# Performance work log

Measured on AMD Instinct MI355X. Metric: run time of the kernel, lower is better.

The kernel has to match this reference:

```python
import jax, jax.numpy as jnp
import numpy as np

EPS = 1e-9
TOP_K = 2


def setup_inputs() -> dict:
    key = jax.random.key(0)
    k = jax.random.split(key, 6)
    B, E, D_IN, D_MODEL, D_SEL = 16384, 8, 900, 512, 128
    return {
        "cycle_curve_data": jax.random.normal(k[0], (B, D_IN), jnp.float32),
        "logits": jax.random.normal(k[1], (B, E), jnp.float32),
        "moe_masks": jax.random.randint(k[2], (B, E), 0, 2, jnp.int32),
        "selection_embeddings": jax.random.normal(k[3], (B, E, D_SEL), jnp.float32),
        "W": jax.random.normal(k[4], (E, D_IN, D_MODEL), jnp.float32) / np.sqrt(D_IN).astype(np.float32),
        "b": jnp.zeros((E, D_MODEL), jnp.float32),
    }


def reference(cycle_curve_data, logits, moe_masks, selection_embeddings, W, b):
    B, E = logits.shape
    mask = (moe_masks == 1).astype(logits.dtype)  # [B, E]
    raw = jax.nn.softmax(logits, axis=1)          # [B, E]

    # inactive-expert mixture for selection embedding
    inactive = raw * (1.0 - mask)
    inactive = inactive / (jnp.sum(inactive, axis=1, keepdims=True) + EPS)
    selection_embedding = jnp.einsum("bes,be->bs", selection_embeddings, inactive)

    # active gates + top-k selection + renormalization
    active = raw * mask
    _, idx = jax.lax.top_k(active, TOP_K)                                  # [B, K]
    top_mask = jnp.sum(jax.nn.one_hot(idx, E, dtype=active.dtype), axis=1)  # [B, E]
    gates = active * top_mask
    gates = gates / (jnp.sum(gates, axis=1, keepdims=True) + EPS)

    # dense formulation of dispatch -> per-expert Linear -> weighted combine:
    # out[b] = sum_e gates[b,e] * (x[b] @ W[e] + b[e])
    expert_out = jnp.einsum("bd,edm->bem", cycle_curve_data, W) + b  # [B, E, D_model]
    final_out = jnp.einsum("bem,be->bm", expert_out, gates).astype(jnp.bfloat16)

    # guide loss (training-mode auxiliary loss)
    s = jnp.sum(raw * mask) / B
    guide_loss = (1.0 - s) * (1.0 - s)
    return final_out, guide_loss, selection_embedding
```

## Files before the change

### kernel.cpp

```cpp
#include <hip/hip_runtime.h>
#include <hip/hip_bf16.h>


#define B_ROWS 16384
#define DIN 900
#define DM 512
#define DSEL 128
#define KP 928
#define NKS 29
#define MAXT 192
#define EPSF 1e-9f

#define OUT_GUIDE (B_ROWS*DM)
#define OUT_SEL   (B_ROWS*DM + 1)

#define WS_COUNTS 0
#define WS_PART   512
#define WS_NT     768
#define WS_OFF    1024
#define WS_ENT    2048
#define WS_BB     9216
#define WS_PIDLR  25600
#define WS_GATEB  91136
#define WS_W8     222208
#define WS_ROWSS  746496
#define WS_WT     812032

#define FRSTRIDE 14848

typedef __attribute__((ext_vector_type(8))) short short8;
typedef __attribute__((ext_vector_type(8))) unsigned short ushort8;
typedef __attribute__((ext_vector_type(4))) float floatx4;

__device__ inline unsigned short f2bf(float v){
  union { __hip_bfloat16 h; unsigned short u; } c;
  c.h = __float2bfloat16(v);
  return c.u;
}
__device__ inline float bf2f(unsigned short u){
  union { unsigned int i; float f; } c;
  c.i = ((unsigned int)u) << 16;
  return c.f;
}
__device__ inline ushort8 pack8u(float4 a, float4 b){
  ushort8 c;
  c[0]=f2bf(a.x); c[1]=f2bf(a.y); c[2]=f2bf(a.z); c[3]=f2bf(a.w);
  c[4]=f2bf(b.x); c[5]=f2bf(b.y); c[6]=f2bf(b.z); c[7]=f2bf(b.w);
  return c;
}

__global__ __launch_bounds__(256) void cvtw2_k(const float* __restrict__ W,
                                               unsigned short* __restrict__ wt2){
  __shared__ unsigned short lds[32][512];
  int t = threadIdx.x;
  int kc = blockIdx.x, e = blockIdx.y;
  for (int kk = 0; kk < 32; ++kk){
    int k = kc*32 + kk;
    if (k < DIN){
      const float* wr = W + ((size_t)e*DIN + k)*DM;
      lds[kk][t]       = f2bf(wr[t]);
      lds[kk][t + 256] = f2bf(wr[t + 256]);
    } else {
      lds[kk][t] = 0; lds[kk][t + 256] = 0;
    }
  }
  __syncthreads();
  int ncg = t >> 3, q = t & 7;
  unsigned short* ob = wt2 + (((size_t)e*32 + ncg)*29 + kc)*512;
  for (int i = 0; i < 8; ++i){
    int fb = i*64 + q*8;
    int col = fb >> 5, kk0 = fb & 31;
    ushort8 y;
    #pragma unroll
    for (int j = 0; j < 8; ++j) y[j] = lds[kk0 + j][ncg*16 + col];
    *((ushort8*)(ob + fb)) = y;
  }
}

__global__ __launch_bounds__(256) void gating_k(const float* __restrict__ logits,
                                                const int* __restrict__ masks,
                                                int* __restrict__ counts,
                                                float* __restrict__ partials,
                                                int* __restrict__ pidlr,
                                                float2* __restrict__ gatesb,
                                                float* __restrict__ w8,
                                                int* __restrict__ blockbase){
  __shared__ int hist[64];
  __shared__ float wsum[4];
  int t = threadIdx.x;
  if (t < 64) hist[t] = 0;
  __syncthreads();
  int b = blockIdx.x*256 + t;
  float4 l0 = *(const float4*)&logits[(size_t)b*8];
  float4 l1 = *(const float4*)&logits[(size_t)b*8 + 4];
  int4  m0 = *(const int4*)&masks[(size_t)b*8];
  int4  m1 = *(const int4*)&masks[(size_t)b*8 + 4];
  float raw[8] = {l0.x,l0.y,l0.z,l0.w,l1.x,l1.y,l1.z,l1.w};
  int   mk[8]  = {m0.x,m0.y,m0.z,m0.w,m1.x,m1.y,m1.z,m1.w};
  float mx = raw[0];
  for (int e = 1; e < 8; e++) mx = fmaxf(mx, raw[e]);
  float Z = 0.f;
  for (int e = 0; e < 8; e++){ raw[e] = expf(raw[e]-mx); Z += raw[e]; }
  float invZ = 1.f/Z;
  float act[8], ina[8]; float srm = 0.f, isum = 0.f;
  for (int e = 0; e < 8; e++){
    raw[e] *= invZ;
    if (mk[e] == 1){ act[e] = raw[e]; ina[e] = 0.f; srm += raw[e]; }
    else           { act[e] = 0.f;    ina[e] = raw[e]; isum += raw[e]; }
  }
  float v1 = -1.f, v2 = -1.f; int e1 = 0, e2 = 0;
  for (int e = 0; e < 8; e++){
    float a = act[e];
    if (a > v1){ v2 = v1; e2 = e1; v1 = a; e1 = e; }
    else if (a > v2){ v2 = a; e2 = e; }
  }
  float den = v1 + v2 + EPSF;
  float g1 = v1/den, g2 = v2/den;
  int lo, hi; float gl, gh;
  if (e1 < e2){ lo = e1; hi = e2; gl = g1; gh = g2; }
  else        { lo = e2; hi = e1; gl = g2; gh = g1; }
  int pid = lo*8 + hi;
  float invI = 1.f/(isum + EPSF);
  for (int e = 0; e < 8; e++) w8[(size_t)b*8 + e] = ina[e]*invI;
  gatesb[b] = make_float2(gl, gh);
  int lr = atomicAdd(&hist[pid], 1);
  pidlr[b] = pid | (lr << 8);
  float s = srm;
  for (int sft = 32; sft > 0; sft >>= 1) s += __shfl_down(s, sft, 64);
  if ((t & 63) == 0) wsum[t >> 6] = s;
  __syncthreads();
  if (t < 64){
    int c = hist[t];
    int base = 0;
    if (c > 0) base = atomicAdd(&counts[t], c);
    blockbase[blockIdx.x*64 + t] = base;
  }
  if (t == 0) partials[blockIdx.x] = wsum[0] + wsum[1] + wsum[2] + wsum[3];
}

__global__ __launch_bounds__(256) void selemb_k(const float* __restrict__ sel,
                                                const float* __restrict__ w8,
                                                const int* __restrict__ pidlr,
                                                const int* __restrict__ off,
                                                const int* __restrict__ blockbase,
                                                int* __restrict__ rows_s,
                                                float* __restrict__ out){
  int t = threadIdx.x;
  int b = blockIdx.x*2 + (t >> 7);
  int d = t & 127;
  if (d == 0){
    int pl = pidlr[b];
    int p = pl & 63;
    int lr = pl >> 8;
    rows_s[off[p] + blockbase[(b >> 8)*64 + p] + lr] = b;
  }
  const float* wr = w8 + (size_t)b*8;
  const float* sb = sel + (size_t)b*(8*DSEL);
  float a = 0.f;
  for (int e = 0; e < 8; e++) a += wr[e] * sb[e*DSEL + d];
  out[OUT_SEL + (size_t)b*DSEL + d] = a;
}

__global__ void worklist_k(const int* __restrict__ counts,
                           const float* __restrict__ partials,
                           int* __restrict__ off, int* __restrict__ ntp,
                           int4* __restrict__ entries,
                           float* __restrict__ out){
  int lane = threadIdx.x;
  int c = counts[lane];
  int sc = c;
  for (int s = 1; s < 64; s <<= 1){ int v = __shfl_up(sc, s, 64); if (lane >= s) sc += v; }
  int offp = sc - c;
  off[lane] = offp;
  int nt = (c + 127) >> 7;
  int snt = nt;
  for (int s = 1; s < 64; s <<= 1){ int v = __shfl_up(snt, s, 64); if (lane >= s) snt += v; }
  int tbase = snt - nt;
  int elo = lane >> 3, ehi = lane & 7;
  for (int j = 0; j < nt; ++j){
    int nr = c - j*128; if (nr > 128) nr = 128;
    entries[tbase + j] = make_int4(elo, ehi, offp + j*128, nr);
  }
  int tot = __shfl(snt, 63, 64);
  if (lane == 0) *ntp = tot;
  float p = partials[lane];
  for (int s = 32; s > 0; s >>= 1) p += __shfl_down(p, s, 64);
  if (lane == 0){
    float sv = p * (1.f/B_ROWS);
    float d = 1.f - sv;
    out[OUT_GUIDE] = d*d;
  }
}


#define ALOADV(P, kk) { \
  const float4* p_ = (const float4*)(xrow + (kk)*32); \
  P##0 = p_[0]; P##1 = p_[1]; P##2 = p_[2]; P##3 = p_[3]; }

#define ALOADT(P) { \
  float tmp[16]; \
  _Pragma("unroll") \
  for (int j = 0; j < 16; ++j){ \
    int k = 896 + skc*16 + j; \
    tmp[j] = (k < DIN) ? xrow[28*32 + j] : 0.f; \
  } \
  P##0 = make_float4(tmp[0],tmp[1],tmp[2],tmp[3]); \
  P##1 = make_float4(tmp[4],tmp[5],tmp[6],tmp[7]); \
  P##2 = make_float4(tmp[8],tmp[9],tmp[10],tmp[11]); \
  P##3 = make_float4(tmp[12],tmp[13],tmp[14],tmp[15]); }

#define AWR(buf, P) { \
  *((ushort8*)&as_[buf][srow*36 + skc*16])     = pack8u(P##0, P##1); \
  *((ushort8*)&as_[buf][srow*36 + skc*16 + 8]) = pack8u(P##2, P##3); }

#define MFJ(j) { \
  acc[0][0][j] = __builtin_amdgcn_mfma_f32_16x16x32_bf16(af0, b0c, acc[0][0][j], 0, 0, 0); \
  acc[0][1][j] = __builtin_amdgcn_mfma_f32_16x16x32_bf16(af1, b0c, acc[0][1][j], 0, 0, 0); \
  acc[0][2][j] = __builtin_amdgcn_mfma_f32_16x16x32_bf16(af2, b0c, acc[0][2][j], 0, 0, 0); \
  acc[0][3][j] = __builtin_amdgcn_mfma_f32_16x16x32_bf16(af3, b0c, acc[0][3][j], 0, 0, 0); \
  acc[1][0][j] = __builtin_amdgcn_mfma_f32_16x16x32_bf16(af0, b1c, acc[1][0][j], 0, 0, 0); \
  acc[1][1][j] = __builtin_amdgcn_mfma_f32_16x16x32_bf16(af1, b1c, acc[1][1][j], 0, 0, 0); \
  acc[1][2][j] = __builtin_amdgcn_mfma_f32_16x16x32_bf16(af2, b1c, acc[1][2][j], 0, 0, 0); \
  acc[1][3][j] = __builtin_amdgcn_mfma_f32_16x16x32_bf16(af3, b1c, acc[1][3][j], 0, 0, 0); }

#define KSTEP(ks, cur, LAST) { \
  short8 af0 = *((const short8*)&as_[cur][(wrow*64 +  0 + l16)*36 + quad*8]); \
  short8 af1 = *((const short8*)&as_[cur][(wrow*64 + 16 + l16)*36 + quad*8]); \
  short8 af2 = *((const short8*)&as_[cur][(wrow*64 + 32 + l16)*36 + quad*8]); \
  short8 af3 = *((const short8*)&as_[cur][(wrow*64 + 48 + l16)*36 + quad*8]); \
  short8 b0n, b1n; \
  b0n = *((const short8*)(bp0 + 1*FRSTRIDE + (size_t)(ks)*512)); \
  b1n = *((const short8*)(bp1 + 1*FRSTRIDE + (size_t)(ks)*512)); \
  MFJ(0); b0c = b0n; b1c = b1n; \
  b0n = *((const short8*)(bp0 + 2*FRSTRIDE + (size_t)(ks)*512)); \
  b1n = *((const short8*)(bp1 + 2*FRSTRIDE + (size_t)(ks)*512)); \
  MFJ(1); b0c = b0n; b1c = b1n; \
  b0n = *((const short8*)(bp0 + 3*FRSTRIDE + (size_t)(ks)*512)); \
  b1n = *((const short8*)(bp1 + 3*FRSTRIDE + (size_t)(ks)*512)); \
  MFJ(2); b0c = b0n; b1c = b1n; \
  if (!(LAST)){ \
    b0n = *((const short8*)(bp0 + (size_t)((ks)+1)*512)); \
    b1n = *((const short8*)(bp1 + (size_t)((ks)+1)*512)); \
  } \
  MFJ(3); b0c = b0n; b1c = b1n; }

__global__ __launch_bounds__(256, 2) void gemm_k(const float* __restrict__ xf,
                                                 const unsigned short* __restrict__ wt2,
                                                 const float* __restrict__ bias,
                                                 const int* __restrict__ ntp,
                                                 const int4* __restrict__ entries,
                                                 const int* __restrict__ rows_s,
                                                 const float2* __restrict__ gatesb,
                                                 float* __restrict__ out){
  int id = blockIdx.x;
  int tile = (id >> 5)*8 + (id & 7);
  int y = (id >> 3) & 3;
  if (tile >= *ntp) return;
  int4 ent = entries[tile];
  int elo = ent.x, ehi = ent.y, start = ent.z, nrows = ent.w;

  __shared__ __align__(16) unsigned short as_[2][128*36];
  __shared__ int   gidx_s[128];
  __shared__ float glo_s[128];
  __shared__ float ghi_s[128];

  int t = threadIdx.x;
  if (t < 128){
    if (t < nrows){
      int g = rows_s[start + t];
      gidx_s[t] = g;
      float2 gg = gatesb[g];
      glo_s[t] = gg.x; ghi_s[t] = gg.y;
    } else { gidx_s[t] = -1; glo_s[t] = 0.f; ghi_s[t] = 0.f; }
  }
  __syncthreads();

  int lane = t & 63, wid = t >> 6;
  int wrow = wid >> 1, wcol = wid & 1;
  int quad = lane >> 4, l16 = lane & 15;
  int ncg0 = y*8 + wcol*4;

  int srow = t >> 1, skc = t & 1;
  int sg = gidx_s[srow];
  const float* xrow = xf + (size_t)(sg >= 0 ? sg : 0)*DIN + skc*16;

  const unsigned short* bp0 = wt2 + ((size_t)(elo*32 + ncg0))*FRSTRIDE + l16*32 + quad*8;
  const unsigned short* bp1 = wt2 + ((size_t)(ehi*32 + ncg0))*FRSTRIDE + l16*32 + quad*8;

  floatx4 acc[2][4][4];
  #pragma unroll
  for (int i = 0; i < 2; i++)
    #pragma unroll
    for (int j = 0; j < 4; j++)
      #pragma unroll
      for (int k = 0; k < 4; k++)
        #pragma unroll
        for (int r = 0; r < 4; r++) acc[i][j][k][r] = 0.f;

  float4 rE0, rE1, rE2, rE3;
  float4 rO0, rO1, rO2, rO3;

  ALOADV(rE, 0);
  ALOADV(rO, 1);
  AWR(0, rE);
  short8 b0c = *((const short8*)(bp0));
  short8 b1c = *((const short8*)(bp1));
  __syncthreads();

  for (int ks = 0; ks < 28; ks += 2){
    if (ks < 26){ ALOADV(rE, ks+2); } else { ALOADT(rE); }
    KSTEP(ks, 0, false);
    AWR(1, rO);
    __syncthreads();
    if (ks < 26){ ALOADV(rO, ks+3); }
    KSTEP(ks+1, 1, false);
    AWR(0, rE);
    __syncthreads();
  }
  KSTEP(28, 0, true);

  int colbase = y*128 + wcol*64;
  float blo[4], bhi[4];
  #pragma unroll
  for (int nt = 0; nt < 4; ++nt){
    int n = colbase + nt*16 + l16;
    blo[nt] = bias[elo*DM + n];
    bhi[nt] = bias[ehi*DM + n];
  }
  #pragma unroll
  for (int mt = 0; mt < 4; ++mt){
    #pragma unroll
    for (int r = 0; r < 4; ++r){
      int rr = wrow*64 + mt*16 + quad*4 + r;
      int grow = gidx_s[rr];
      if (grow >= 0){
        float2 gg = gatesb[grow];
        float* orow = out + (size_t)grow*DM;
        #pragma unroll
        for (int nt = 0; nt < 4; ++nt){
          int n = colbase + nt*16 + l16;
          float v = gg.x*(acc[0][mt][nt][r] + blo[nt]) + gg.y*(acc[1][mt][nt][r] + bhi[nt]);
          orow[n] = bf2f(f2bf(v));
        }
      }
    }
  }
}

extern "C" void kernel_launch(void* const* d_in, const int* in_sizes, int n_in,
                              void* d_out, int out_size, void* d_ws, size_t ws_size,
                              hipStream_t stream){
  const float* x      = (const float*)d_in[0];
  const float* logits = (const float*)d_in[1];
  const int*   masks  = (const int*)d_in[2];
  const float* sel    = (const float*)d_in[3];
  const float* W      = (const float*)d_in[4];
  const float* bias   = (const float*)d_in[5];
  float* out = (float*)d_out;
  char* ws = (char*)d_ws;
  int*    counts   = (int*)(ws + WS_COUNTS);
  float*  partials = (float*)(ws + WS_PART);
  int*    ntp      = (int*)(ws + WS_NT);
  int*    off      = (int*)(ws + WS_OFF);
  int4*   entries  = (int4*)(ws + WS_ENT);
  int*    blockbase= (int*)(ws + WS_BB);
  int*    pidlr    = (int*)(ws + WS_PIDLR);
  float2* gatesb   = (float2*)(ws + WS_GATEB);
  float*  w8       = (float*)(ws + WS_W8);
  int*    rows_s   = (int*)(ws + WS_ROWSS);
  unsigned short* wt2 = (unsigned short*)(ws + WS_WT);

  hipMemsetAsync(ws, 0, 256, stream);
  cvtw2_k<<<dim3(29, 8), 256, 0, stream>>>(W, wt2);
  gating_k<<<B_ROWS/256, 256, 0, stream>>>(logits, masks, counts, partials, pidlr, gatesb, w8, blockbase);
  worklist_k<<<1, 64, 0, stream>>>(counts, partials, off, ntp, entries, out);
  selemb_k<<<B_ROWS/2, 256, 0, stream>>>(sel, w8, pidlr, off, blockbase, rows_s, out);
  gemm_k<<<4*MAXT, 256, 0, stream>>>(x, wt2, bias, ntp, entries, rows_s, gatesb, out);
}
```

Measured before the change: 324.8 us.

## Fuse weight-convert and gating kernels, scan counts serially, stage B tiles through LDS

Weight conversion and gating now run as one kernel, which removes a launch and the memset. The global atomic counters are replaced by per-block histograms that the worklist kernel prefix-scans serially. The GEMM now loads its weight fragments cooperatively into double-buffered LDS instead of each wave reading them directly from global memory, so loads are coalesced and shared across the waves of a block. The cost is extra LDS use, which may limit occupancy, and a longer serial scan in the single worklist block.

```diff
diff --git a/kernel.cpp b/kernel.cpp
--- a/kernel.cpp
+++ b/kernel.cpp
@@ -26,8 +26,6 @@
 #define WS_ROWSS  746496
 #define WS_WT     812032
 
-#define FRSTRIDE 14848
-
 typedef __attribute__((ext_vector_type(8))) short short8;
 typedef __attribute__((ext_vector_type(8))) unsigned short ushort8;
 typedef __attribute__((ext_vector_type(4))) float floatx4;
@@ -49,48 +47,49 @@
   return c;
 }
 
-__global__ __launch_bounds__(256) void cvtw2_k(const float* __restrict__ W,
-                                               unsigned short* __restrict__ wt2){
+__global__ __launch_bounds__(256) void prep_k(const float* __restrict__ W,
+                                              unsigned short* __restrict__ wt2,
+                                              const float* __restrict__ logits,
+                                              const int* __restrict__ masks,
+                                              float* __restrict__ partials,
+                                              int* __restrict__ pidlr,
+                                              float2* __restrict__ gatesb,
+                                              float* __restrict__ w8,
+                                              int* __restrict__ blockbase){
   __shared__ unsigned short lds[32][512];
-  int t = threadIdx.x;
-  int kc = blockIdx.x, e = blockIdx.y;
-  for (int kk = 0; kk < 32; ++kk){
-    int k = kc*32 + kk;
-    if (k < DIN){
-      const float* wr = W + ((size_t)e*DIN + k)*DM;
-      lds[kk][t]       = f2bf(wr[t]);
-      lds[kk][t + 256] = f2bf(wr[t + 256]);
-    } else {
-      lds[kk][t] = 0; lds[kk][t + 256] = 0;
-    }
-  }
-  __syncthreads();
-  int ncg = t >> 3, q = t & 7;
-  unsigned short* ob = wt2 + (((size_t)e*32 + ncg)*29 + kc)*512;
-  for (int i = 0; i < 8; ++i){
-    int fb = i*64 + q*8;
-    int col = fb >> 5, kk0 = fb & 31;
-    ushort8 y;
-    #pragma unroll
-    for (int j = 0; j < 8; ++j) y[j] = lds[kk0 + j][ncg*16 + col];
-    *((ushort8*)(ob + fb)) = y;
-  }
-}
-
-__global__ __launch_bounds__(256) void gating_k(const float* __restrict__ logits,
-                                                const int* __restrict__ masks,
-                                                int* __restrict__ counts,
-                                                float* __restrict__ partials,
-                                                int* __restrict__ pidlr,
-                                                float2* __restrict__ gatesb,
-                                                float* __restrict__ w8,
-                                                int* __restrict__ blockbase){
   __shared__ int hist[64];
   __shared__ float wsum[4];
   int t = threadIdx.x;
+  int bid = blockIdx.x;
+  if (bid < 232){
+    int kc = bid % 29, e = bid / 29;
+    for (int kk = 0; kk < 32; ++kk){
+      int k = kc*32 + kk;
+      if (k < DIN){
+        const float* wr = W + ((size_t)e*DIN + k)*DM;
+        lds[kk][t]       = f2bf(wr[t]);
+        lds[kk][t + 256] = f2bf(wr[t + 256]);
+      } else {
+        lds[kk][t] = 0; lds[kk][t + 256] = 0;
+      }
+    }
+    __syncthreads();
+    int ncg = t >> 3, q = t & 7;
+    unsigned short* ob = wt2 + (((size_t)e*32 + ncg)*29 + kc)*512;
+    for (int i = 0; i < 8; ++i){
+      int fb = i*64 + q*8;
+      int col = fb >> 5, kk0 = fb & 31;
+      ushort8 y;
+      #pragma unroll
+      for (int j = 0; j < 8; ++j) y[j] = lds[kk0 + j][ncg*16 + col];
+      *((ushort8*)(ob + fb)) = y;
+    }
+    return;
+  }
+  int gb = bid - 232;
   if (t < 64) hist[t] = 0;
   __syncthreads();
-  int b = blockIdx.x*256 + t;
+  int b = gb*256 + t;
   float4 l0 = *(const float4*)&logits[(size_t)b*8];
   float4 l1 = *(const float4*)&logits[(size_t)b*8 + 4];
   int4  m0 = *(const int4*)&masks[(size_t)b*8];
@@ -129,13 +128,47 @@
   for (int sft = 32; sft > 0; sft >>= 1) s += __shfl_down(s, sft, 64);
   if ((t & 63) == 0) wsum[t >> 6] = s;
   __syncthreads();
-  if (t < 64){
-    int c = hist[t];
-    int base = 0;
-    if (c > 0) base = atomicAdd(&counts[t], c);
-    blockbase[blockIdx.x*64 + t] = base;
-  }
-  if (t == 0) partials[blockIdx.x] = wsum[0] + wsum[1] + wsum[2] + wsum[3];
+  if (t < 64) blockbase[gb*64 + t] = hist[t];
+  if (t == 0) partials[gb] = wsum[0] + wsum[1] + wsum[2] + wsum[3];
+}
+
+__global__ void worklist_k(int* __restrict__ blockbase,
+                           const float* __restrict__ partials,
+                           int* __restrict__ off, int* __restrict__ ntp,
+                           int4* __restrict__ entries,
+                           float* __restrict__ out){
+  int lane = threadIdx.x;
+  int s = 0;
+  for (int b0 = 0; b0 < 64; b0 += 16){
+    int v[16];
+    #pragma unroll
+    for (int j = 0; j < 16; ++j) v[j] = blockbase[(b0+j)*64 + lane];
+    #pragma unroll
+    for (int j = 0; j < 16; ++j){ blockbase[(b0+j)*64 + lane] = s; s += v[j]; }
+  }
+  int c = s;
+  int sc = c;
+  for (int sh = 1; sh < 64; sh <<= 1){ int v = __shfl_up(sc, sh, 64); if (lane >= sh) sc += v; }
+  int offp = sc - c;
+  off[lane] = offp;
+  int nt = (c + 127) >> 7;
+  int snt = nt;
+  for (int sh = 1; sh < 64; sh <<= 1){ int v = __shfl_up(snt, sh, 64); if (lane >= sh) snt += v; }
+  int tbase = snt - nt;
+  int elo = lane >> 3, ehi = lane & 7;
+  for (int j = 0; j < nt; ++j){
+    int nr = c - j*128; if (nr > 128) nr = 128;
+    entries[tbase + j] = make_int4(elo, ehi, offp + j*128, nr);
+  }
+  int tot = __shfl(snt, 63, 64);
+  if (lane == 0) *ntp = tot;
+  float p = partials[lane];
+  for (int sh = 32; sh > 0; sh >>= 1) p += __shfl_down(p, sh, 64);
+  if (lane == 0){
+    float sv = p * (1.f/B_ROWS);
+    float d = 1.f - sv;
+    out[OUT_GUIDE] = d*d;
+  }
 }
 
 __global__ __launch_bounds__(256) void selemb_k(const float* __restrict__ sel,
@@ -161,37 +194,6 @@
   out[OUT_SEL + (size_t)b*DSEL + d] = a;
 }
 
-__global__ void worklist_k(const int* __restrict__ counts,
-                           const float* __restrict__ partials,
-                           int* __restrict__ off, int* __restrict__ ntp,
-                           int4* __restrict__ entries,
-                           float* __restrict__ out){
-  int lane = threadIdx.x;
-  int c = counts[lane];
-  int sc = c;
-  for (int s = 1; s < 64; s <<= 1){ int v = __shfl_up(sc, s, 64); if (lane >= s) sc += v; }
-  int offp = sc - c;
-  off[lane] = offp;
-  int nt = (c + 127) >> 7;
-  int snt = nt;
-  for (int s = 1; s < 64; s <<= 1){ int v = __shfl_up(snt, s, 64); if (lane >= s) snt += v; }
-  int tbase = snt - nt;
-  int elo = lane >> 3, ehi = lane & 7;
-  for (int j = 0; j < nt; ++j){
-    int nr = c - j*128; if (nr > 128) nr = 128;
-    entries[tbase + j] = make_int4(elo, ehi, offp + j*128, nr);
-  }
-  int tot = __shfl(snt, 63, 64);
-  if (lane == 0) *ntp = tot;
-  float p = partials[lane];
-  for (int s = 32; s > 0; s >>= 1) p += __shfl_down(p, s, 64);
-  if (lane == 0){
-    float sv = p * (1.f/B_ROWS);
-    float d = 1.f - sv;
-    out[OUT_GUIDE] = d*d;
-  }
-}
-
 
 #define ALOADV(P, kk) { \
   const float4* p_ = (const float4*)(xrow + (kk)*32); \
@@ -213,36 +215,34 @@
   *((ushort8*)&as_[buf][srow*36 + skc*16])     = pack8u(P##0, P##1); \
   *((ushort8*)&as_[buf][srow*36 + skc*16 + 8]) = pack8u(P##2, P##3); }
 
-#define MFJ(j) { \
-  acc[0][0][j] = __builtin_amdgcn_mfma_f32_16x16x32_bf16(af0, b0c, acc[0][0][j], 0, 0, 0); \
-  acc[0][1][j] = __builtin_amdgcn_mfma_f32_16x16x32_bf16(af1, b0c, acc[0][1][j], 0, 0, 0); \
-  acc[0][2][j] = __builtin_amdgcn_mfma_f32_16x16x32_bf16(af2, b0c, acc[0][2][j], 0, 0, 0); \
-  acc[0][3][j] = __builtin_amdgcn_mfma_f32_16x16x32_bf16(af3, b0c, acc[0][3][j], 0, 0, 0); \
-  acc[1][0][j] = __builtin_amdgcn_mfma_f32_16x16x32_bf16(af0, b1c, acc[1][0][j], 0, 0, 0); \
-  acc[1][1][j] = __builtin_amdgcn_mfma_f32_16x16x32_bf16(af1, b1c, acc[1][1][j], 0, 0, 0); \
-  acc[1][2][j] = __builtin_amdgcn_mfma_f32_16x16x32_bf16(af2, b1c, acc[1][2][j], 0, 0, 0); \
-  acc[1][3][j] = __builtin_amdgcn_mfma_f32_16x16x32_bf16(af3, b1c, acc[1][3][j], 0, 0, 0); }
-
-#define KSTEP(ks, cur, LAST) { \
+#define BLOADG(kk) { \
+  bw0 = *((const ushort8*)(bgp0 + (size_t)(kk)*512)); \
+  bw1 = *((const ushort8*)(bgp1 + (size_t)(kk)*512)); \
+  bw2 = *((const ushort8*)(bgp2 + (size_t)(kk)*512)); \
+  bw3 = *((const ushort8*)(bgp3 + (size_t)(kk)*512)); }
+
+#define BWR(buf) { \
+  *((ushort8*)&bs_[buf][bo0]) = bw0; \
+  *((ushort8*)&bs_[buf][bo1]) = bw1; \
+  *((ushort8*)&bs_[buf][bo2]) = bw2; \
+  *((ushort8*)&bs_[buf][bo3]) = bw3; }
+
+#define KSTEP(cur) { \
   short8 af0 = *((const short8*)&as_[cur][(wrow*64 +  0 + l16)*36 + quad*8]); \
   short8 af1 = *((const short8*)&as_[cur][(wrow*64 + 16 + l16)*36 + quad*8]); \
   short8 af2 = *((const short8*)&as_[cur][(wrow*64 + 32 + l16)*36 + quad*8]); \
   short8 af3 = *((const short8*)&as_[cur][(wrow*64 + 48 + l16)*36 + quad*8]); \
-  short8 b0n, b1n; \
-  b0n = *((const short8*)(bp0 + 1*FRSTRIDE + (size_t)(ks)*512)); \
-  b1n = *((const short8*)(bp1 + 1*FRSTRIDE + (size_t)(ks)*512)); \
-  MFJ(0); b0c = b0n; b1c = b1n; \
-  b0n = *((const short8*)(bp0 + 2*FRSTRIDE + (size_t)(ks)*512)); \
-  b1n = *((const short8*)(bp1 + 2*FRSTRIDE + (size_t)(ks)*512)); \
-  MFJ(1); b0c = b0n; b1c = b1n; \
-  b0n = *((const short8*)(bp0 + 3*FRSTRIDE + (size_t)(ks)*512)); \
-  b1n = *((const short8*)(bp1 + 3*FRSTRIDE + (size_t)(ks)*512)); \
-  MFJ(2); b0c = b0n; b1c = b1n; \
-  if (!(LAST)){ \
-    b0n = *((const short8*)(bp0 + (size_t)((ks)+1)*512)); \
-    b1n = *((const short8*)(bp1 + (size_t)((ks)+1)*512)); \
-  } \
-  MFJ(3); b0c = b0n; b1c = b1n; }
+  _Pragma("unroll") \
+  for (int e = 0; e < 2; ++e){ \
+    _Pragma("unroll") \
+    for (int nt = 0; nt < 4; ++nt){ \
+      short8 bfr = *((const short8*)&bs_[cur][(e*8 + wcol*4 + nt)*512 + quad*128 + l16*8]); \
+      acc[e][0][nt] = __builtin_amdgcn_mfma_f32_16x16x32_bf16(af0, bfr, acc[e][0][nt], 0, 0, 0); \
+      acc[e][1][nt] = __builtin_amdgcn_mfma_f32_16x16x32_bf16(af1, bfr, acc[e][1][nt], 0, 0, 0); \
+      acc[e][2][nt] = __builtin_amdgcn_mfma_f32_16x16x32_bf16(af2, bfr, acc[e][2][nt], 0, 0, 0); \
+      acc[e][3][nt] = __builtin_amdgcn_mfma_f32_16x16x32_bf16(af3, bfr, acc[e][3][nt], 0, 0, 0); \
+    } \
+  } }
 
 __global__ __launch_bounds__(256, 2) void gemm_k(const float* __restrict__ xf,
                                                  const unsigned short* __restrict__ wt2,
@@ -260,6 +260,7 @@
   int elo = ent.x, ehi = ent.y, start = ent.z, nrows = ent.w;
 
   __shared__ __align__(16) unsigned short as_[2][128*36];
+  __shared__ __align__(16) unsigned short bs_[2][16*512];
   __shared__ int   gidx_s[128];
   __shared__ float glo_s[128];
   __shared__ float ghi_s[128];
@@ -278,14 +279,24 @@
   int lane = t & 63, wid = t >> 6;
   int wrow = wid >> 1, wcol = wid & 1;
   int quad = lane >> 4, l16 = lane & 15;
-  int ncg0 = y*8 + wcol*4;
 
   int srow = t >> 1, skc = t & 1;
   int sg = gidx_s[srow];
   const float* xrow = xf + (size_t)(sg >= 0 ? sg : 0)*DIN + skc*16;
 
-  const unsigned short* bp0 = wt2 + ((size_t)(elo*32 + ncg0))*FRSTRIDE + l16*32 + quad*8;
-  const unsigned short* bp1 = wt2 + ((size_t)(ehi*32 + ncg0))*FRSTRIDE + l16*32 + quad*8;
+  const unsigned short *bgp0, *bgp1, *bgp2, *bgp3;
+  int bo0, bo1, bo2, bo3;
+  {
+    int v = t & 63;
+    int goff = v*8;
+    int lofs = (v & 3)*128 + (v >> 2)*8;
+    int g0 = t >> 6, g1 = (256+t) >> 6, g2 = (512+t) >> 6, g3 = (768+t) >> 6;
+    bgp0 = wt2 + ((size_t)((g0 < 8 ? elo : ehi)*32 + y*8 + (g0 & 7))*29)*512 + goff;
+    bgp1 = wt2 + ((size_t)((g1 < 8 ? elo : ehi)*32 + y*8 + (g1 & 7))*29)*512 + goff;
+    bgp2 = wt2 + ((size_t)((g2 < 8 ? elo : ehi)*32 + y*8 + (g2 & 7))*29)*512 + goff;
+    bgp3 = wt2 + ((size_t)((g3 < 8 ? elo : ehi)*32 + y*8 + (g3 & 7))*29)*512 + goff;
+    bo0 = g0*512 + lofs; bo1 = g1*512 + lofs; bo2 = g2*512 + lofs; bo3 = g3*512 + lofs;
+  }
 
   floatx4 acc[2][4][4];
   #pragma unroll
@@ -299,25 +310,27 @@
 
   float4 rE0, rE1, rE2, rE3;
   float4 rO0, rO1, rO2, rO3;
+  ushort8 bw0, bw1, bw2, bw3;
 
   ALOADV(rE, 0);
   ALOADV(rO, 1);
-  AWR(0, rE);
-  short8 b0c = *((const short8*)(bp0));
-  short8 b1c = *((const short8*)(bp1));
+  BLOADG(0);
+  AWR(0, rE); BWR(0);
   __syncthreads();
 
   for (int ks = 0; ks < 28; ks += 2){
     if (ks < 26){ ALOADV(rE, ks+2); } else { ALOADT(rE); }
-    KSTEP(ks, 0, false);
-    AWR(1, rO);
+    BLOADG(ks+1);
+    KSTEP(0);
+    AWR(1, rO); BWR(1);
     __syncthreads();
     if (ks < 26){ ALOADV(rO, ks+3); }
-    KSTEP(ks+1, 1, false);
-    AWR(0, rE);
+    BLOADG(ks+2);
+    KSTEP(1);
+    AWR(0, rE); BWR(0);
     __syncthreads();
   }
-  KSTEP(28, 0, true);
+  KSTEP(0);
 
   int colbase = y*128 + wcol*64;
   float blo[4], bhi[4];
@@ -358,7 +371,6 @@
   const float* bias   = (const float*)d_in[5];
   float* out = (float*)d_out;
   char* ws = (char*)d_ws;
-  int*    counts   = (int*)(ws + WS_COUNTS);
   float*  partials = (float*)(ws + WS_PART);
   int*    ntp      = (int*)(ws + WS_NT);
   int*    off      = (int*)(ws + WS_OFF);
@@ -370,10 +382,8 @@
   int*    rows_s   = (int*)(ws + WS_ROWSS);
   unsigned short* wt2 = (unsigned short*)(ws + WS_WT);
 
-  hipMemsetAsync(ws, 0, 256, stream);
-  cvtw2_k<<<dim3(29, 8), 256, 0, stream>>>(W, wt2);
-  gating_k<<<B_ROWS/256, 256, 0, stream>>>(logits, masks, counts, partials, pidlr, gatesb, w8, blockbase);
-  worklist_k<<<1, 64, 0, stream>>>(counts, partials, off, ntp, entries, out);
+  prep_k<<<296, 256, 0, stream>>>(W, wt2, logits, masks, partials, pidlr, gatesb, w8, blockbase);
+  worklist_k<<<1, 64, 0, stream>>>(blockbase, partials, off, ntp, entries, out);
   selemb_k<<<B_ROWS/2, 256, 0, stream>>>(sel, w8, pidlr, off, blockbase, rows_s, out);
   gemm_k<<<4*MAXT, 256, 0, stream>>>(x, wt2, bias, ntp, entries, rows_s, gatesb, out);
 }
```

Result: faster. 274.0 us (-15.6%).
